# Performance work log

Hardware: AMD Instinct MI355X
Metric: run time of the kernel (lower is better)

Reference implementation:

```python
import math
import jax, jax.numpy as jnp
import numpy as np

B, S, HIDDEN = 1, 8192, 2048
NUM_HEADS = 16
HEAD_DIM = HIDDEN // NUM_HEADS
NUM_FW = 4
FW_DIM = HIDDEN // NUM_FW
D_H = FW_DIM  # inter_multi = 1.0
WINDOW = 256
CHUNK = 2048
ROPE_THETA = 500000.0
BASE_LR_INV = float(np.log(np.expm1(0.001)))  # inv_softplus(1e-3)


def rms_norm(x, w, eps=1e-6):
    return x * jax.lax.rsqrt(jnp.mean(x * x, axis=-1, keepdims=True) + eps) * w


def apply_rope(q, k, theta):
    D = q.shape[-1]
    inv = 1.0 / (theta ** (jnp.arange(0, D, 2, dtype=jnp.float32) / D))
    t = jnp.arange(q.shape[1], dtype=jnp.float32)
    f = t[:, None] * inv[None, :]  # [S, D/2]
    cos = jnp.cos(f)[None, :, None, :]
    sin = jnp.sin(f)[None, :, None, :]
    def ap(x):
        x1, x2 = jnp.split(x, 2, axis=-1)
        return jnp.concatenate([x1 * cos - x2 * sin, x2 * cos + x1 * sin], axis=-1)
    return ap(q), ap(k)


def sliding_window_attn(q, k, v, window):
    # q,k,v: [B,S,H,D]; causal window of `window` tokens incl. self (flash (window-1, 0))
    B_, S_, H_, D_ = q.shape
    W = window
    nc = S_ // W
    def blk(x):
        return x.transpose(0, 2, 1, 3).reshape(B_, H_, nc, W, D_)
    qb, kb, vb = blk(q), blk(k), blk(v)
    pad = jnp.zeros((B_, H_, 1, W, D_), q.dtype)
    k2 = jnp.concatenate([jnp.concatenate([pad, kb[:, :, :-1]], 2), kb], 3)  # [B,H,nc,2W,D]
    v2 = jnp.concatenate([jnp.concatenate([pad, vb[:, :, :-1]], 2), vb], 3)
    r = jnp.arange(W)[:, None]
    j = jnp.arange(2 * W)[None, :]
    base = (j >= r + 1) & (j <= W + r)  # causal + within-window
    keypos = (jnp.arange(nc)[:, None, None] - 1) * W + j[None]
    mask = base[None] & (keypos >= 0)  # [nc,W,2W]
    scores = jnp.einsum('bhnqd,bhnkd->bhnqk', qb, k2) * (1.0 / math.sqrt(D_))
    scores = jnp.where(mask[None, None], scores, -jnp.inf)
    p = jax.nn.softmax(scores, axis=-1)
    o = jnp.einsum('bhnqk,bhnkd->bhnqd', p, v2)
    return o.reshape(B_, H_, S_, D_).transpose(0, 2, 1, 3)


def ttt_swiglu(fq, fk, fv, l0, l1, l2, w0, w1, w2, chunk):
    # fq/fk/fv: [BN,S,d]; l*: [BN,S,1]; w0,w2: [BN,dh,d]; w1: [BN,d,dh]
    BN, S_, d = fq.shape
    nc = S_ // chunk
    def ch(x):
        return x.reshape(BN, nc, chunk, x.shape[-1]).transpose(1, 0, 2, 3)
    xs = (ch(fq), ch(fk), ch(fv), ch(l0), ch(l1), ch(l2))
    def step(carry, x):
        w0c, w1c, w2c = carry
        qi, ki, vi, lr0, lr1, lr2 = x
        # apply current fast weights to chunk queries (SwiGLU MLP)
        o = jnp.einsum('bch,boh->bco',
                       jax.nn.silu(jnp.einsum('bcd,bhd->bch', qi, w0c)) * jnp.einsum('bcd,bhd->bch', qi, w2c),
                       w1c)
        # manual gradient of dot-product TTT loss L = -sum(v * f(k))
        g = jnp.einsum('bcd,bhd->bch', ki, w0c)
        hm = jnp.einsum('bcd,bhd->bch', ki, w2c)
        sg = jax.nn.sigmoid(g)
        silu_g = g * sg
        hid = silu_g * hm
        dhid = jnp.einsum('bco,boh->bch', vi, w1c)
        dhm = dhid * silu_g
        dg = dhid * hm
        dgp = dg * (sg * (1.0 + g * (1.0 - sg)))  # silu backprop
        w0n = w0c + jnp.einsum('bch,bcd->bhd', dgp * lr0, ki)
        w2n = w2c + jnp.einsum('bch,bcd->bhd', dhm * lr2, ki)
        w1n = w1c + jnp.einsum('bco,bch->boh', vi * lr1, hid)
        return (w0n, w1n, w2n), o
    _, outs = jax.lax.scan(step, (w0, w1, w2), xs)
    return outs.transpose(1, 0, 2, 3).reshape(BN, S_, d)


def setup_inputs():
    key = jax.random.key(0)
    ks = jax.random.split(key, 8)
    h = HIDDEN
    return {
        'hidden_states': jax.random.normal(ks[0], (B, S, h), jnp.float32),
        'qkv_w': jax.random.normal(ks[1], (3 * h, h), jnp.float32) * 0.02,
        'q_norm_w': jnp.ones((h,), jnp.float32),
        'k_norm_w': jnp.ones((h,), jnp.float32),
        'qk_scale': jnp.ones((h, 2), jnp.float32),
        'qk_offset': jnp.zeros((h, 2), jnp.float32),
        'lr_w': jax.random.normal(ks[2], (3 * NUM_FW, h), jnp.float32) * 0.02,
        'lr_b': jnp.zeros((3 * NUM_FW,), jnp.float32),
        'w0': jax.random.normal(ks[3], (NUM_FW, D_H, FW_DIM), jnp.float32) / math.sqrt(FW_DIM),
        'w1': jax.random.normal(ks[4], (NUM_FW, FW_DIM, D_H), jnp.float32) / math.sqrt(D_H),
        'w2': jax.random.normal(ks[5], (NUM_FW, D_H, FW_DIM), jnp.float32) / math.sqrt(FW_DIM),
        'ttt_norm_w': jnp.ones((FW_DIM,), jnp.float32),
        'o_proj_w': jax.random.normal(ks[6], (h, h), jnp.float32) * 0.02,
    }


def reference(hidden_states, qkv_w, q_norm_w, k_norm_w, qk_scale, qk_offset,
              lr_w, lr_b, w0, w1, w2, ttt_norm_w, o_proj_w):
    qkv = hidden_states @ qkv_w.T
    q, k, v = jnp.split(qkv, 3, axis=-1)
    q = rms_norm(q, q_norm_w)
    k = rms_norm(k, k_norm_w)
    # rescale q/k for the fast-weight path
    fq = q * qk_scale[:, 0] + qk_offset[:, 0]
    fk = k * qk_scale[:, 1] + qk_offset[:, 1]
    fv = v
    # windowed RoPE attention path
    qh = q.reshape(B, S, NUM_HEADS, HEAD_DIM)
    kh = k.reshape(B, S, NUM_HEADS, HEAD_DIM)
    vh = v.reshape(B, S, NUM_HEADS, HEAD_DIM)
    qh, kh = apply_rope(qh, kh, ROPE_THETA)
    attn_o = sliding_window_attn(qh, kh, vh, WINDOW).reshape(B, S, HIDDEN)
    # fast-weight (TTT) path: silu + per-head l2-norm on q/k
    fq = jax.nn.silu(fq).reshape(B, S, NUM_FW, FW_DIM)
    fk = jax.nn.silu(fk).reshape(B, S, NUM_FW, FW_DIM)
    fv = jax.nn.silu(fv).reshape(B, S, NUM_FW, FW_DIM)
    fq = fq / jnp.maximum(jnp.linalg.norm(fq, axis=-1, keepdims=True), 1e-12)
    fk = fk / jnp.maximum(jnp.linalg.norm(fk, axis=-1, keepdims=True), 1e-12)
    def flat(x):
        return x.transpose(0, 2, 1, 3).reshape(B * NUM_FW, S, FW_DIM)
    # per-token learning rates (mamba parameterization)
    lr = jax.nn.softplus(hidden_states @ lr_w.T + lr_b + BASE_LR_INV)  # [B,S,3*NH]
    l0, l1, l2 = jnp.split(lr, 3, axis=-1)
    def flat_lr(x):
        return x.transpose(0, 2, 1).reshape(B * NUM_FW, S, 1)
    def bcast(w):
        return jnp.broadcast_to(w[None], (B,) + w.shape).reshape(B * NUM_FW, w.shape[1], w.shape[2])
    o_fast = ttt_swiglu(flat(fq), flat(fk), flat(fv),
                        flat_lr(l0), flat_lr(l1), flat_lr(l2),
                        bcast(w0), bcast(w1), bcast(w2), CHUNK)
    o_fast = rms_norm(o_fast.reshape(B, NUM_FW, S, FW_DIM), ttt_norm_w)
    o_fast = o_fast.transpose(0, 2, 1, 3).reshape(B, S, HIDDEN)
    return (attn_o + o_fast) @ o_proj_w.T
```

## Files before the change

kernel.cpp:

```cpp
#include <hip/hip_runtime.h>
#include <hip/hip_bf16.h>

typedef __hip_bfloat16 bf16;
typedef __bf16 bft;
typedef bft bf16x8 __attribute__((ext_vector_type(8)));
typedef bft bf16x4 __attribute__((ext_vector_type(4)));
typedef float f32x4 __attribute__((ext_vector_type(4)));

#define S_LEN 8192
#define HID   2048
#define QKV3  6144
#define NH    16
#define HD    128
#define NFW   4
#define FD    512
#define CHUNK_LEN 2048
#define NCHUNK 4
#define BASE_LR_INV (-6.9072552f)
#define QKP 136
#define VSP 72
#define PSP 76

__device__ __forceinline__ float bf2f(bf16 x){ return __bfloat162float(x); }
__device__ __forceinline__ bf16  f2bf(float x){ return __float2bfloat16(x); }
__device__ __forceinline__ float sigm(float x){ return 1.f/(1.f+__expf(-x)); }
__device__ __forceinline__ float siluf(float x){ return x/(1.f+__expf(-x)); }
__device__ __forceinline__ float wave_sum(float v){
  #pragma unroll
  for(int off=32; off; off>>=1) v += __shfl_xor(v, off, 64);
  return v;
}

template<int ROWS, typename T>
__device__ __forceinline__ void stage(const T* __restrict__ src, long ld,
                                      bft* dst, int tid)
{
  if constexpr (sizeof(T) == 2) {
    const int lane = tid & 63, wv = tid >> 6;
    #pragma unroll
    for (int i = 0; i < ROWS/64; ++i) {
      const int r0 = wv*16 + i*64;
      const int row = r0 + (lane >> 2);
      const int g = (lane & 3) ^ ((row >> 1) & 3);
      const bft* gp = (const bft*)src + (size_t)row*ld + g*8;
      bft* lp = dst + (size_t)r0*32;
      __builtin_amdgcn_global_load_lds(
          (const __attribute__((address_space(1))) void*)gp,
          (__attribute__((address_space(3))) void*)lp, 16, 0, 0);
    }
  } else {
    #pragma unroll
    for (int i = 0; i < ROWS/64; ++i) {
      const int e = tid + i*256;
      const int row = e >> 2, c = e & 3;
      const int g = c ^ ((row >> 1) & 3);
      const float* sp = (const float*)src + (size_t)row*ld + g*8;
      const float4 v0 = *(const float4*)sp;
      const float4 v1 = *(const float4*)(sp + 4);
      bf16x8 b;
      b[0]=(bft)v0.x; b[1]=(bft)v0.y; b[2]=(bft)v0.z; b[3]=(bft)v0.w;
      b[4]=(bft)v1.x; b[5]=(bft)v1.y; b[6]=(bft)v1.z; b[7]=(bft)v1.w;
      *(bf16x8*)(dst + (size_t)row*32 + c*8) = b;
    }
  }
}

template<int BM,int BN,int EPI, typename TA, typename TB>
__global__ __launch_bounds__(256) void mgemm_k(
    const TA* __restrict__ A, const TB* __restrict__ B, void* __restrict__ Cv,
    bft* __restrict__ Ct, int K, long lda, long ldb, long ldc,
    long sA, long sB, long sC)
{
  constexpr int AM = BM/32, AN = BN/32;
  __shared__ __align__(16) bft As[BM*32];
  __shared__ __align__(16) bft Bs[BN*32];
  const int tid = threadIdx.x;
  const int z = blockIdx.z;
  A += (size_t)z * sA;
  B += (size_t)z * sB;
  const size_t m0 = (size_t)blockIdx.y * BM, n0 = (size_t)blockIdx.x * BN;
  const int wv = tid >> 6, lane = tid & 63;
  const int wm = (wv & 1) * (BM/2), wn = (wv >> 1) * (BN/2);
  const int fr = lane & 15;
  const int fsw = ((lane >> 4) ^ ((fr >> 1) & 3)) * 8;

  f32x4 acc[AM][AN];
  #pragma unroll
  for (int i=0;i<AM;i++)
    #pragma unroll
    for (int j=0;j<AN;j++) acc[i][j] = (f32x4){0.f,0.f,0.f,0.f};

  const TA* Ab = A + m0*lda;
  const TB* Bb = B + n0*ldb;
  for (int kt = 0; kt < K; kt += 32) {
    __syncthreads();
    stage<BM>(Ab + kt, lda, As, tid);
    stage<BN>(Bb + kt, ldb, Bs, tid);
    __syncthreads();
    bf16x8 af[AM], bfv[AN];
    #pragma unroll
    for (int mi=0; mi<AM; mi++)
      af[mi] = *(const bf16x8*)(As + (size_t)(wm + mi*16 + fr)*32 + fsw);
    #pragma unroll
    for (int ni=0; ni<AN; ni++)
      bfv[ni] = *(const bf16x8*)(Bs + (size_t)(wn + ni*16 + fr)*32 + fsw);
    #pragma unroll
    for (int mi=0; mi<AM; mi++)
      #pragma unroll
      for (int ni=0; ni<AN; ni++)
        acc[mi][ni] = __builtin_amdgcn_mfma_f32_16x16x32_bf16(af[mi], bfv[ni], acc[mi][ni], 0, 0, 0);
  }

  const int er = (lane >> 4) * 4;
  const int ec = lane & 15;
  #pragma unroll
  for (int mi=0; mi<AM; mi++){
    #pragma unroll
    for (int ni=0; ni<AN; ni++){
      #pragma unroll
      for (int r=0; r<4; r++){
        size_t row = m0 + wm + mi*16 + er + r;
        size_t col = n0 + wn + ni*16 + ec;
        size_t idx = (size_t)z*sC + row*ldc + col;
        float v = acc[mi][ni][r];
        if constexpr (EPI == 0){
          ((bft*)Cv)[idx] = (bft)v;
        } else if constexpr (EPI == 1){
          ((float*)Cv)[idx] = v;
        } else {
          float nv = ((float*)Cv)[idx] + v;
          ((float*)Cv)[idx] = nv;
          if (Ct) Ct[(size_t)z*FD*FD + col*FD + row] = (bft)nv;
        }
      }
    }
  }
}

template<int BM,int BN,int EPI, typename TA, typename TB>
static inline void mgemm(hipStream_t st, const TA* A, const TB* B, void* C, bft* Ct,
    int M, int N, int K, long lda, long ldb, long ldc,
    int batch, long sA, long sB, long sC)
{
  dim3 g(N/BN, M/BM, batch);
  mgemm_k<BM,BN,EPI,TA,TB><<<g, 256, 0, st>>>(A, B, C, Ct, K, lda, ldb, ldc, sA, sB, sC);
}

__device__ __forceinline__ void stage8(const bft* __restrict__ src, long ld,
                                       bft* dst, int tid)
{
  const int lane = tid & 63, wv = tid >> 6;
  #pragma unroll
  for (int i = 0; i < 2; ++i) {
    const int r0 = wv*16 + i*128;
    const int row = r0 + (lane >> 2);
    const int g = (lane & 3) ^ ((row >> 1) & 3);
    const bft* gp = src + (size_t)row*ld + g*8;
    bft* lp = dst + (size_t)r0*32;
    __builtin_amdgcn_global_load_lds(
        (const __attribute__((address_space(1))) void*)gp,
        (__attribute__((address_space(3))) void*)lp, 16, 0, 0);
  }
}

template<int EPI>
__global__ __launch_bounds__(512, 2) void mgemm8_k(
    const bft* __restrict__ A, const bft* __restrict__ B, void* __restrict__ Cv,
    int K, long lda, long ldb, long ldc)
{
  __shared__ __align__(16) bft As[4][256*32];
  __shared__ __align__(16) bft Bs[4][256*32];
  const int tid = threadIdx.x;

  const int gx = (int)gridDim.x;
  const int nwg = (int)(gridDim.x * gridDim.y);
  int lin = (int)(blockIdx.y * gridDim.x + blockIdx.x);
  if ((nwg & 7) == 0) lin = (lin & 7) * (nwg >> 3) + (lin >> 3);
  const size_t m0 = (size_t)(lin / gx) * 256;
  const size_t n0 = (size_t)(lin % gx) * 256;

  const int wv = tid >> 6, lane = tid & 63;
  const int wm = (wv & 1) * 128, wn = (wv >> 1) * 64;
  const int fr = lane & 15;
  const int fsw = ((lane >> 4) ^ ((fr >> 1) & 3)) * 8;

  f32x4 acc[8][4];
  #pragma unroll
  for (int i=0;i<8;i++)
    #pragma unroll
    for (int j=0;j<4;j++) acc[i][j] = (f32x4){0.f,0.f,0.f,0.f};

  const bft* Ab = A + m0*lda;
  const bft* Bb = B + n0*ldb;
  const int NS = K >> 5;

  stage8(Ab,      lda, As[0], tid);
  stage8(Bb,      ldb, Bs[0], tid);
  stage8(Ab + 32, lda, As[1], tid);
  stage8(Bb + 32, ldb, Bs[1], tid);

  auto compute = [&](int s){
    const bft* Ap = As[s & 3];
    const bft* Bp = Bs[s & 3];
    bf16x8 af[8], bv[4];
    #pragma unroll
    for (int mi=0; mi<8; mi++)
      af[mi] = *(const bf16x8*)(Ap + (size_t)(wm + mi*16 + fr)*32 + fsw);
    #pragma unroll
    for (int ni=0; ni<4; ni++)
      bv[ni] = *(const bf16x8*)(Bp + (size_t)(wn + ni*16 + fr)*32 + fsw);
    __builtin_amdgcn_s_setprio(1);
    #pragma unroll
    for (int mi=0; mi<8; mi++)
      #pragma unroll
      for (int ni=0; ni<4; ni++)
        acc[mi][ni] = __builtin_amdgcn_mfma_f32_16x16x32_bf16(af[mi], bv[ni], acc[mi][ni], 0, 0, 0);
    __builtin_amdgcn_s_setprio(0);
  };

  for (int s = 0; s < NS - 2; ++s) {
    const int kt = (s + 2) * 32;
    stage8(Ab + kt, lda, As[(s+2)&3], tid);
    stage8(Bb + kt, ldb, Bs[(s+2)&3], tid);
    asm volatile("s_waitcnt vmcnt(8)" ::: "memory");
    __builtin_amdgcn_s_barrier();
    asm volatile("" ::: "memory");
    compute(s);
  }
  asm volatile("s_waitcnt vmcnt(4)" ::: "memory");
  __builtin_amdgcn_s_barrier();
  asm volatile("" ::: "memory");
  compute(NS - 2);
  asm volatile("s_waitcnt vmcnt(0)" ::: "memory");
  __builtin_amdgcn_s_barrier();
  asm volatile("" ::: "memory");
  compute(NS - 1);

  const int er = (lane >> 4) * 4;
  const int ec = lane & 15;
  #pragma unroll
  for (int mi=0; mi<8; mi++){
    #pragma unroll
    for (int ni=0; ni<4; ni++){
      #pragma unroll
      for (int r=0; r<4; r++){
        size_t row = m0 + wm + mi*16 + er + r;
        size_t col = n0 + wn + ni*16 + ec;
        size_t idx = row*ldc + col;
        float v = acc[mi][ni][r];
        if constexpr (EPI == 0) ((bft*)Cv)[idx] = (bft)v;
        else                    ((float*)Cv)[idx] = v;
      }
    }
  }
}

template<int EPI>
static inline void mgemm8(hipStream_t st, const bft* A, const bft* B, void* C,
                          int M, int N, int K, long lda, long ldb, long ldc)
{
  dim3 g(N/256, M/256, 1);
  mgemm8_k<EPI><<<g, 512, 0, st>>>(A, B, C, K, lda, ldb, ldc);
}

__global__ __launch_bounds__(256) void cvt_k(const float* __restrict__ s,
    bft* __restrict__ d)
{
  size_t i = ((size_t)blockIdx.x*256 + threadIdx.x) * 8;
  const float4 v0 = *(const float4*)(s + i);
  const float4 v1 = *(const float4*)(s + i + 4);
  bf16x8 b;
  b[0]=(bft)v0.x; b[1]=(bft)v0.y; b[2]=(bft)v0.z; b[3]=(bft)v0.w;
  b[4]=(bft)v1.x; b[5]=(bft)v1.y; b[6]=(bft)v1.z; b[7]=(bft)v1.w;
  *(bf16x8*)(d + i) = b;
}

__global__ __launch_bounds__(256) void tr_k(const bft* __restrict__ in,
    bft* __restrict__ out, long ldin, long sIn, long sOut)
{
  __shared__ __align__(16) bft t[64][72];
  const int c0 = blockIdx.x*64, r0 = blockIdx.y*64;
  in  += (size_t)blockIdx.z * sIn;
  out += (size_t)blockIdx.z * sOut;
  const int tid = threadIdx.x;
  #pragma unroll
  for (int i=0;i<2;i++){
    int e = tid + i*256;
    int r = e >> 3, c8 = (e & 7) * 8;
    *(bf16x8*)&t[r][c8] = *(const bf16x8*)(in + (size_t)(r0+r)*ldin + c0 + c8);
  }
  __syncthreads();
  #pragma unroll
  for (int i=0;i<2;i++){
    int e = tid + i*256;
    int c = e >> 3, r8 = (e & 7) * 8;
    bf16x8 v;
    #pragma unroll
    for (int j=0;j<8;j++) v[j] = t[r8+j][c];
    *(bf16x8*)(out + (size_t)(c0+c)*CHUNK_LEN + r0 + r8) = v;
  }
}

__global__ __launch_bounds__(256) void tcw1_k(const float* __restrict__ w1,
    bft* __restrict__ w1tb)
{
  size_t idx = (size_t)blockIdx.x*256 + threadIdx.x;
  int z = (int)(idx >> 18);
  int h = (int)((idx >> 9) & 511);
  int o = (int)(idx & 511);
  w1tb[idx] = (bft)w1[(size_t)z*FD*FD + (size_t)o*FD + h];
}

__global__ __launch_bounds__(256) void vt_k(const bf16* __restrict__ qkv,
    bft* __restrict__ vT)
{
  __shared__ __align__(16) bft t[64*QKP];
  const int s0 = blockIdx.x * 64;
  const int h  = blockIdx.y;
  const int tid = threadIdx.x;
  #pragma unroll
  for (int i=0;i<4;i++){
    int e = tid + i*256;
    int rr = e >> 4, doff = (e & 15) * 8;
    *(bf16x8*)(t + rr*QKP + doff) =
        *(const bf16x8*)((const bft*)qkv + (size_t)(s0+rr)*QKV3 + 2*HID + h*HD + doff);
  }
  __syncthreads();
  #pragma unroll
  for (int it=0; it<4; it++){
    int d = (tid >> 3) + it*32;
    int so8 = (tid & 7) * 8;
    bf16x8 v;
    #pragma unroll
    for (int j=0;j<8;j++) v[j] = t[(so8+j)*QKP + d];
    *(bf16x8*)(vT + ((size_t)(h*HD + d))*S_LEN + s0 + so8) = v;
  }
}

__global__ void rope_k(float* __restrict__ rc, float* __restrict__ rs){
  int pos = blockIdx.x, d = threadIdx.x;
  float inv = 1.f / powf(500000.0f, (float)d * (1.0f/64.0f));
  float ang = (float)pos * inv;
  rc[pos*64+d] = cosf(ang);
  rs[pos*64+d] = sinf(ang);
}

__global__ __launch_bounds__(256) void lr_k(const float* __restrict__ hidden,
    const float* __restrict__ lr_w, const float* __restrict__ lr_b,
    float* __restrict__ lro)
{
  __shared__ float hrow[HID];
  __shared__ float red[4][12];
  int s = blockIdx.x, tid = threadIdx.x;
  for(int i=0;i<HID/256;i++) hrow[tid+256*i] = hidden[(size_t)s*HID + tid + 256*i];
  __syncthreads();
  float part[12];
  #pragma unroll
  for(int o=0;o<12;o++) part[o]=0.f;
  for(int i=0;i<HID/256;i++){
    int j = tid + 256*i;
    float h = hrow[j];
    #pragma unroll
    for(int o=0;o<12;o++) part[o] += h * lr_w[o*HID + j];
  }
  int lane = tid & 63, w = tid >> 6;
  #pragma unroll
  for(int o=0;o<12;o++){
    float v = wave_sum(part[o]);
    if(lane==0) red[w][o] = v;
  }
  __syncthreads();
  if(tid < 12){
    float v = red[0][tid]+red[1][tid]+red[2][tid]+red[3][tid] + lr_b[tid] + BASE_LR_INV;
    float sp = (v > 20.f) ? v : log1pf(expf(v));
    lro[s*12 + tid] = sp;
  }
}

__global__ __launch_bounds__(256) void e2a_k(
    bf16* __restrict__ qkv,
    const float* __restrict__ qnw, const float* __restrict__ knw)
{
  __shared__ float red[8];
  int s = blockIdx.x, tid = threadIdx.x;
  int lane = tid & 63, w = tid >> 6;
  float qv[8], kv[8];
  float sq = 0.f, sk = 0.f;
  size_t base = (size_t)s*QKV3;
  #pragma unroll
  for(int i=0;i<8;i++){
    int j = tid*8 + i;
    qv[i] = bf2f(qkv[base + j]);
    kv[i] = bf2f(qkv[base + HID + j]);
    sq += qv[i]*qv[i]; sk += kv[i]*kv[i];
  }
  sq = wave_sum(sq); sk = wave_sum(sk);
  if(lane==0){ red[w] = sq; red[4+w] = sk; }
  __syncthreads();
  float rq = rsqrtf((red[0]+red[1]+red[2]+red[3])*(1.f/HID) + 1e-6f);
  float rk = rsqrtf((red[4]+red[5]+red[6]+red[7])*(1.f/HID) + 1e-6f);
  #pragma unroll
  for(int i=0;i<8;i++){
    int j = tid*8 + i;
    qkv[base + j]       = f2bf(qv[i]*rq*qnw[j]);
    qkv[base + HID + j] = f2bf(kv[i]*rk*knw[j]);
  }
}

__global__ __launch_bounds__(256) void e2b_k(
    bf16* __restrict__ qkv,
    const float* __restrict__ qks, const float* __restrict__ qko)
{
  int s = blockIdx.x, tid = threadIdx.x;
  size_t base = (size_t)s*QKV3;
  float a[8], b[8], vv[8];
  float ga = 0.f, gb2 = 0.f;
  #pragma unroll
  for(int i=0;i<8;i++){
    int j = tid*8 + i;
    float qn = bf2f(qkv[base + j]);
    float kn = bf2f(qkv[base + HID + j]);
    float v  = bf2f(qkv[base + 2*HID + j]);
    a[i] = siluf(qn*qks[2*j]   + qko[2*j]);
    b[i] = siluf(kn*qks[2*j+1] + qko[2*j+1]);
    vv[i] = siluf(v);
    ga += a[i]*a[i]; gb2 += b[i]*b[i];
  }
  ga = wave_sum(ga); gb2 = wave_sum(gb2);
  float iq = 1.f / fmaxf(sqrtf(ga), 1e-12f);
  float ik = 1.f / fmaxf(sqrtf(gb2), 1e-12f);
  #pragma unroll
  for(int i=0;i<8;i++){
    int j = tid*8 + i;
    qkv[base + j]         = f2bf(a[i]*iq);
    qkv[base + HID + j]   = f2bf(b[i]*ik);
    qkv[base + 2*HID + j] = f2bf(vv[i]);
  }
}

__global__ __launch_bounds__(256) void attn_k(
    const bf16* __restrict__ qkv, const bft* __restrict__ vT,
    const float* __restrict__ rc, const float* __restrict__ rs,
    float* __restrict__ attn)
{
  __shared__ __align__(16) bft Qs[64*QKP];
  __shared__ __align__(16) bft Ks[64*QKP];
  __shared__ __align__(16) bft Vs[128*VSP];
  __shared__ __align__(16) bft Ps[64*PSP];
  const int head = blockIdx.x >> 7;
  const int Q0 = (blockIdx.x & 127) * 64;
  const int tid = threadIdx.x;
  const int hb = head * HD;
  const int lane = tid & 63;
  const int wm = (tid >> 6) * 16;
  const int fr = lane & 15, fko = (lane >> 4) * 8;
  const int rbase = (lane >> 4) * 4;

  #pragma unroll
  for(int i=0;i<16;i++){
    int e = tid + i*256;
    int rr = e >> 6, d = e & 63;
    int qpos = Q0 + rr;
    size_t b = (size_t)qpos*QKV3 + hb;
    float x1 = bf2f(qkv[b + d]);
    float x2 = bf2f(qkv[b + d + 64]);
    float c = rc[qpos*64 + d], sn = rs[qpos*64 + d];
    Qs[rr*QKP + d]      = (bft)(x1*c - x2*sn);
    Qs[rr*QKP + d + 64] = (bft)(x2*c + x1*sn);
  }
  __syncthreads();
  bf16x8 qf[4];
  #pragma unroll
  for (int kk=0;kk<4;kk++)
    qf[kk] = *(const bf16x8*)(Qs + (wm+fr)*QKP + kk*32 + fko);

  f32x4 Ot[8];
  #pragma unroll
  for (int i=0;i<8;i++) Ot[i] = (f32x4){0.f,0.f,0.f,0.f};
  float m4[4], l4[4];
  #pragma unroll
  for (int r=0;r<4;r++){ m4[r] = -INFINITY; l4[r] = 0.f; }

  for (int kt=0; kt<5; kt++){
    const int kb = Q0 - 256 + kt*64;
    if (kb < 0) continue;
    __syncthreads();
    #pragma unroll
    for(int i=0;i<16;i++){
      int e = tid + i*256;
      int rr = e >> 6, d = e & 63;
      int kpos = kb + rr;
      size_t b = (size_t)kpos*QKV3 + HID + hb;
      float x1 = bf2f(qkv[b + d]);
      float x2 = bf2f(qkv[b + d + 64]);
      float c = rc[kpos*64 + d], sn = rs[kpos*64 + d];
      Ks[rr*QKP + d]      = (bft)(x1*c - x2*sn);
      Ks[rr*QKP + d + 64] = (bft)(x2*c + x1*sn);
    }
    {
      int d = tid >> 1, koff = (tid & 1) * 32;
      const bft* vrow = vT + ((size_t)(hb + d))*S_LEN + kb + koff;
      bft* lrow = Vs + d*VSP + koff;
      #pragma unroll
      for (int j8=0;j8<4;j8++)
        *(bf16x8*)(lrow + j8*8) = *(const bf16x8*)(vrow + j8*8);
    }
    __syncthreads();

    f32x4 st[4];
    #pragma unroll
    for (int nt=0;nt<4;nt++){
      f32x4 acc = (f32x4){0.f,0.f,0.f,0.f};
      #pragma unroll
      for (int kk=0;kk<4;kk++){
        bf16x8 kf = *(const bf16x8*)(Ks + (nt*16+fr)*QKP + kk*32 + fko);
        acc = __builtin_amdgcn_mfma_f32_16x16x32_bf16(qf[kk], kf, acc, 0, 0, 0);
      }
      st[nt] = acc;
    }

    float pv[4][4];
    #pragma unroll
    for (int r=0;r<4;r++){
      int qpos = Q0 + wm + rbase + r;
      float sm[4];
      float mx = -INFINITY;
      #pragma unroll
      for (int nt=0;nt<4;nt++){
        int kpos = kb + nt*16 + fr;
        bool valid = (kpos > qpos - 256) && (kpos <= qpos);
        float s = valid ? st[nt][r] * 0.088388347648318447f : -INFINITY;
        sm[nt] = s;
        mx = fmaxf(mx, s);
      }
      mx = fmaxf(mx, __shfl_xor(mx, 1, 64));
      mx = fmaxf(mx, __shfl_xor(mx, 2, 64));
      mx = fmaxf(mx, __shfl_xor(mx, 4, 64));
      mx = fmaxf(mx, __shfl_xor(mx, 8, 64));
      float mnew = fmaxf(m4[r], mx);
      float alpha = (mnew == -INFINITY) ? 1.f : __expf(m4[r] - mnew);
      float ps = 0.f;
      #pragma unroll
      for (int nt=0;nt<4;nt++){
        float p = (sm[nt] == -INFINITY) ? 0.f : __expf(sm[nt] - mnew);
        pv[nt][r] = p;
        ps += p;
      }
      ps += __shfl_xor(ps, 1, 64);
      ps += __shfl_xor(ps, 2, 64);
      ps += __shfl_xor(ps, 4, 64);
      ps += __shfl_xor(ps, 8, 64);
      l4[r] = l4[r]*alpha + ps;
      m4[r] = mnew;
      #pragma unroll
      for (int ct=0;ct<8;ct++) Ot[ct][r] *= alpha;
    }

    #pragma unroll
    for (int r=0;r<4;r++){
      int row = wm + rbase + r;
      #pragma unroll
      for (int nt=0;nt<4;nt++)
        Ps[row*PSP + nt*16 + fr] = (bft)pv[nt][r];
    }
    bf16x8 af[2];
    #pragma unroll
    for (int kk=0;kk<2;kk++){
      const bft* pp = Ps + (wm+fr)*PSP + kk*32 + fko;
      bf16x4 lo = *(const bf16x4*)pp;
      bf16x4 hi = *(const bf16x4*)(pp+4);
      bf16x8 a;
      #pragma unroll
      for (int j=0;j<4;j++){ a[j]=lo[j]; a[j+4]=hi[j]; }
      af[kk]=a;
    }
    #pragma unroll
    for (int ct=0;ct<8;ct++)
      #pragma unroll
      for (int kk=0;kk<2;kk++){
        bf16x8 bv = *(const bf16x8*)(Vs + (ct*16+fr)*VSP + kk*32 + fko);
        Ot[ct] = __builtin_amdgcn_mfma_f32_16x16x32_bf16(af[kk], bv, Ot[ct], 0, 0, 0);
      }
  }

  #pragma unroll
  for (int r=0;r<4;r++){
    float invl = 1.f / l4[r];
    int qpos = Q0 + wm + rbase + r;
    size_t ob = (size_t)qpos*HID + hb;
    #pragma unroll
    for (int ct=0;ct<8;ct++)
      attn[ob + ct*16 + fr] = Ot[ct][r] * invl;
  }
}

__global__ __launch_bounds__(256) void e3_k(
    const bf16* __restrict__ g, const bf16* __restrict__ hm,
    bf16* __restrict__ qg, const bf16* __restrict__ qm,
    bf16* __restrict__ hid)
{
  size_t idx = (size_t)blockIdx.x*256 + threadIdx.x;
  float opre = siluf(bf2f(qg[idx])) * bf2f(qm[idx]);
  hid[idx] = f2bf(siluf(bf2f(g[idx])) * bf2f(hm[idx]));
  qg[idx]  = f2bf(opre);
}

__global__ __launch_bounds__(256) void e4_k(
    bf16* __restrict__ g, bf16* __restrict__ hm, bf16* __restrict__ dhid,
    const bf16* __restrict__ qkv, const float* __restrict__ lrb, int cbase)
{
  size_t idx = (size_t)blockIdx.x*256 + threadIdx.x;
  int h  = (int)(idx >> 20);
  int ci = (int)((idx >> 9) & 2047);
  int d  = (int)(idx & 511);
  int s  = cbase + ci;
  float l0  = lrb[s*12 + h];
  float l1  = lrb[s*12 + 4 + h];
  float l2v = lrb[s*12 + 8 + h];
  float gg = bf2f(g[idx]), hv = bf2f(hm[idx]), dh = bf2f(dhid[idx]);
  float sg = sigm(gg);
  float silu_g = gg * sg;
  float dhm = dh * silu_g;
  float dg  = dh * hv;
  float dgp = dg * (sg * (1.f + gg * (1.f - sg)));
  float fvv = bf2f(qkv[(size_t)s*QKV3 + 2*HID + h*FD + d]);
  g[idx]    = f2bf(dgp * l0);
  hm[idx]   = f2bf(dhm * l2v);
  dhid[idx] = f2bf(fvv * l1);
}

__global__ __launch_bounds__(256) void e5_k(const float* __restrict__ attn,
    const bf16* __restrict__ ofc, const float* __restrict__ tnw,
    bf16* __restrict__ qkv, int cbase)
{
  int ci = blockIdx.x, tid = threadIdx.x;
  int s = cbase + ci;
  int lane = tid & 63, w = tid >> 6;
  float o[8]; float ss = 0.f;
  size_t ob = ((size_t)w*CHUNK_LEN + ci)*FD + (size_t)lane*8;
  #pragma unroll
  for(int i=0;i<8;i++){ o[i] = bf2f(ofc[ob+i]); ss += o[i]*o[i]; }
  ss = wave_sum(ss);
  float inv = rsqrtf(ss*(1.f/FD) + 1e-6f);
  size_t xb = (size_t)s*QKV3 + w*FD + (size_t)lane*8;
  size_t ab = (size_t)s*HID  + w*FD + (size_t)lane*8;
  #pragma unroll
  for(int i=0;i<8;i++){
    int d = lane*8 + i;
    qkv[xb+i] = f2bf(attn[ab+i] + o[i]*inv*tnw[d]);
  }
}

extern "C" void kernel_launch(void* const* d_in, const int* in_sizes, int n_in,
                              void* d_out, int out_size, void* d_ws, size_t ws_size,
                              hipStream_t stream)
{
  (void)in_sizes; (void)n_in; (void)out_size;
  const float* hidden   = (const float*)d_in[0];
  const float* qkv_w    = (const float*)d_in[1];
  const float* q_norm_w = (const float*)d_in[2];
  const float* k_norm_w = (const float*)d_in[3];
  const float* qk_scale = (const float*)d_in[4];
  const float* qk_off   = (const float*)d_in[5];
  const float* lr_w     = (const float*)d_in[6];
  const float* lr_b     = (const float*)d_in[7];
  const float* w0_in    = (const float*)d_in[8];
  const float* w1_in    = (const float*)d_in[9];
  const float* w2_in    = (const float*)d_in[10];
  const float* ttt_nw   = (const float*)d_in[11];
  const float* o_proj   = (const float*)d_in[12];
  float* out = (float*)d_out;

  char* p = (char*)d_ws;
  auto alloc = [&](size_t n){ char* r = p; p += (n + 255) & ~(size_t)255; return (void*)r; };

  bf16*  qkv   = (bf16*) alloc((size_t)S_LEN*QKV3*sizeof(bf16));
  float* lrb   = (float*)alloc((size_t)S_LEN*12*sizeof(float));
  float* rc    = (float*)alloc((size_t)S_LEN*64*sizeof(float));
  float* rs    = (float*)alloc((size_t)S_LEN*64*sizeof(float));
  float* w0s   = (float*)alloc((size_t)NFW*FD*FD*sizeof(float));
  float* w1s   = (float*)alloc((size_t)NFW*FD*FD*sizeof(float));
  float* w2s   = (float*)alloc((size_t)NFW*FD*FD*sizeof(float));
  bft*   w1tb  = (bft*)  alloc((size_t)NFW*FD*FD*sizeof(bft));
  bf16*  gb    = (bf16*) alloc((size_t)NFW*CHUNK_LEN*FD*sizeof(bf16));
  bf16*  hmb   = (bf16*) alloc((size_t)NFW*CHUNK_LEN*FD*sizeof(bf16));
  bf16*  qgb   = (bf16*) alloc((size_t)NFW*CHUNK_LEN*FD*sizeof(bf16));
  bf16*  qmb   = (bf16*) alloc((size_t)NFW*CHUNK_LEN*FD*sizeof(bf16));
  bf16*  hidb  = (bf16*) alloc((size_t)NFW*CHUNK_LEN*FD*sizeof(bf16));
  bf16*  ofc   = (bf16*) alloc((size_t)NFW*CHUNK_LEN*FD*sizeof(bf16));
  bft*   fkT   = (bft*)  alloc((size_t)NFW*FD*CHUNK_LEN*sizeof(bft));
  bft*   hidT  = (bft*)  alloc((size_t)NFW*FD*CHUNK_LEN*sizeof(bft));
  bft*   a2T   = (bft*)  alloc((size_t)NFW*FD*CHUNK_LEN*sizeof(bft));
  bft*   a1T   = (bft*)  alloc((size_t)NFW*FD*CHUNK_LEN*sizeof(bft));

  if ((size_t)(p - (char*)d_ws) > ws_size) return;

  bft* hidden_bf = (bft*)gb;
  bft* qkvw_bf   = (bft*)fkT;
  bft* vT        = (bft*)fkT;
  bft* opw_bf    = (bft*)hidb;

  float* attn = out;

  hipMemcpyAsync(w0s, w0_in, (size_t)NFW*FD*FD*sizeof(float), hipMemcpyDeviceToDevice, stream);
  hipMemcpyAsync(w1s, w1_in, (size_t)NFW*FD*FD*sizeof(float), hipMemcpyDeviceToDevice, stream);
  hipMemcpyAsync(w2s, w2_in, (size_t)NFW*FD*FD*sizeof(float), hipMemcpyDeviceToDevice, stream);

  rope_k<<<S_LEN, 64, 0, stream>>>(rc, rs);
  lr_k<<<S_LEN, 256, 0, stream>>>(hidden, lr_w, lr_b, lrb);
  tcw1_k<<<NFW*FD*FD/256, 256, 0, stream>>>(w1_in, w1tb);
  cvt_k<<<(S_LEN*HID)/2048, 256, 0, stream>>>(hidden, hidden_bf);
  cvt_k<<<(QKV3*HID)/2048, 256, 0, stream>>>(qkv_w, qkvw_bf);

  mgemm8<0>(stream, hidden_bf, qkvw_bf, (void*)qkv, S_LEN, QKV3, HID, HID, HID, QKV3);

  e2a_k<<<S_LEN, 256, 0, stream>>>(qkv, q_norm_w, k_norm_w);
  vt_k<<<dim3(S_LEN/64, NH), 256, 0, stream>>>(qkv, vT);
  attn_k<<<NH*128, 256, 0, stream>>>(qkv, vT, rc, rs, attn);
  e2b_k<<<S_LEN, 256, 0, stream>>>(qkv, qk_scale, qk_off);

  const long sW  = (long)FD*FD;
  const long sCh = (long)CHUNK_LEN*FD;
  const long sT  = (long)FD*CHUNK_LEN;
  const int  NEL = NFW*CHUNK_LEN*FD/256;
  const dim3 tg(FD/64, CHUNK_LEN/64, NFW);

  for(int c=0; c<NCHUNK; c++){
    const bft* fqc = (const bft*)qkv + (size_t)c*CHUNK_LEN*QKV3;
    const bft* fkc = fqc + HID;
    const bft* fvc = fqc + 2*HID;
    mgemm<128,128,0>(stream, fkc, w0s, gb,  (bft*)nullptr, CHUNK_LEN, FD, FD, QKV3, FD, FD, NFW, FD, sW, sCh);
    mgemm<128,128,0>(stream, fkc, w2s, hmb, (bft*)nullptr, CHUNK_LEN, FD, FD, QKV3, FD, FD, NFW, FD, sW, sCh);
    mgemm<128,128,0>(stream, fqc, w0s, qgb, (bft*)nullptr, CHUNK_LEN, FD, FD, QKV3, FD, FD, NFW, FD, sW, sCh);
    mgemm<128,128,0>(stream, fqc, w2s, qmb, (bft*)nullptr, CHUNK_LEN, FD, FD, QKV3, FD, FD, NFW, FD, sW, sCh);
    e3_k<<<NEL, 256, 0, stream>>>(gb, hmb, qgb, qmb, hidb);
    mgemm<128,128,0>(stream, (const bft*)qgb, w1s, ofc, (bft*)nullptr, CHUNK_LEN, FD, FD, FD, FD, FD, NFW, sCh, sW, sCh);
    mgemm<128,128,0>(stream, fvc, (const bft*)w1tb, qmb, (bft*)nullptr, CHUNK_LEN, FD, FD, QKV3, FD, FD, NFW, FD, sW, sCh);
    e4_k<<<NEL, 256, 0, stream>>>(gb, hmb, qmb, qkv, lrb, c*CHUNK_LEN);
    tr_k<<<tg, 256, 0, stream>>>(fkc,              fkT,        QKV3, FD,  sT);
    tr_k<<<tg, 256, 0, stream>>>((const bft*)hidb, hidT,       FD,   sCh, sT);
    tr_k<<<tg, 256, 0, stream>>>((const bft*)gb,   (bft*)qgb,  FD,   sCh, sT);
    tr_k<<<tg, 256, 0, stream>>>((const bft*)hmb,  a2T,        FD,   sCh, sT);
    tr_k<<<tg, 256, 0, stream>>>((const bft*)qmb,  a1T,        FD,   sCh, sT);
    mgemm<64,64,2>(stream, (const bft*)qgb, fkT,  w0s, (bft*)nullptr, FD, FD, CHUNK_LEN, CHUNK_LEN, CHUNK_LEN, FD, NFW, sT, sT, sW);
    mgemm<64,64,2>(stream, a2T,             fkT,  w2s, (bft*)nullptr, FD, FD, CHUNK_LEN, CHUNK_LEN, CHUNK_LEN, FD, NFW, sT, sT, sW);
    mgemm<64,64,2>(stream, a1T,             hidT, w1s, w1tb,          FD, FD, CHUNK_LEN, CHUNK_LEN, CHUNK_LEN, FD, NFW, sT, sT, sW);
    e5_k<<<CHUNK_LEN, 256, 0, stream>>>(attn, ofc, ttt_nw, qkv, c*CHUNK_LEN);
  }

  cvt_k<<<(HID*HID)/2048, 256, 0, stream>>>(o_proj, opw_bf);
  mgemm8<1>(stream, (const bft*)qkv, opw_bf, out, S_LEN, HID, HID, QKV3, HID, HID);
}
```

Measured before the change: 1.703 ms.

## Pipeline TTT GEMM loads with 4-stage LDS ring and keep bf16 weight copies

Replaces the single-buffered, double-barrier mgemm loop with a 4-slot LDS ring that prefetches two K-steps ahead using global_load_lds, explicit vmcnt waits and one barrier per step, and raises MFMA issue priority. Fast weights are now also kept as bf16 copies, refreshed in the weight-update epilogue. This lets every GEMM take the async bf16 staging path instead of loading fp32 and converting in registers. The cost is extra bf16 stores in the update epilogue, more LDS per block, and three small conversion kernels.

```diff
diff --git a/kernel.cpp b/kernel.cpp
--- a/kernel.cpp
+++ b/kernel.cpp
@@ -31,49 +31,43 @@
   return v;
 }
 
-template<int ROWS, typename T>
-__device__ __forceinline__ void stage(const T* __restrict__ src, long ld,
+template<int N>
+__device__ __forceinline__ void waitcnt_vm(){
+  static_assert(N==0||N==2||N==4||N==8, "unsupported vmcnt");
+  if constexpr (N==0)      asm volatile("s_waitcnt vmcnt(0)" ::: "memory");
+  else if constexpr (N==2) asm volatile("s_waitcnt vmcnt(2)" ::: "memory");
+  else if constexpr (N==4) asm volatile("s_waitcnt vmcnt(4)" ::: "memory");
+  else                     asm volatile("s_waitcnt vmcnt(8)" ::: "memory");
+}
+
+template<int ROWS>
+__device__ __forceinline__ void stage(const bft* __restrict__ src, long ld,
                                       bft* dst, int tid)
 {
-  if constexpr (sizeof(T) == 2) {
-    const int lane = tid & 63, wv = tid >> 6;
-    #pragma unroll
-    for (int i = 0; i < ROWS/64; ++i) {
-      const int r0 = wv*16 + i*64;
-      const int row = r0 + (lane >> 2);
-      const int g = (lane & 3) ^ ((row >> 1) & 3);
-      const bft* gp = (const bft*)src + (size_t)row*ld + g*8;
-      bft* lp = dst + (size_t)r0*32;
-      __builtin_amdgcn_global_load_lds(
-          (const __attribute__((address_space(1))) void*)gp,
-          (__attribute__((address_space(3))) void*)lp, 16, 0, 0);
-    }
-  } else {
-    #pragma unroll
-    for (int i = 0; i < ROWS/64; ++i) {
-      const int e = tid + i*256;
-      const int row = e >> 2, c = e & 3;
-      const int g = c ^ ((row >> 1) & 3);
-      const float* sp = (const float*)src + (size_t)row*ld + g*8;
-      const float4 v0 = *(const float4*)sp;
-      const float4 v1 = *(const float4*)(sp + 4);
-      bf16x8 b;
-      b[0]=(bft)v0.x; b[1]=(bft)v0.y; b[2]=(bft)v0.z; b[3]=(bft)v0.w;
-      b[4]=(bft)v1.x; b[5]=(bft)v1.y; b[6]=(bft)v1.z; b[7]=(bft)v1.w;
-      *(bf16x8*)(dst + (size_t)row*32 + c*8) = b;
-    }
-  }
-}
-
-template<int BM,int BN,int EPI, typename TA, typename TB>
+  const int lane = tid & 63, wv = tid >> 6;
+  #pragma unroll
+  for (int i = 0; i < ROWS/64; ++i) {
+    const int r0 = wv*16 + i*64;
+    const int row = r0 + (lane >> 2);
+    const int g = (lane & 3) ^ ((row >> 1) & 3);
+    const bft* gp = src + (size_t)row*ld + g*8;
+    bft* lp = dst + (size_t)r0*32;
+    __builtin_amdgcn_global_load_lds(
+        (const __attribute__((address_space(1))) void*)gp,
+        (__attribute__((address_space(3))) void*)lp, 16, 0, 0);
+  }
+}
+
+template<int BM,int BN,int EPI>
 __global__ __launch_bounds__(256) void mgemm_k(
-    const TA* __restrict__ A, const TB* __restrict__ B, void* __restrict__ Cv,
-    bft* __restrict__ Ct, int K, long lda, long ldb, long ldc,
-    long sA, long sB, long sC)
+    const bft* __restrict__ A, const bft* __restrict__ B, void* __restrict__ Cv,
+    bft* __restrict__ Cd, bft* __restrict__ Ct, int K,
+    long lda, long ldb, long ldc, long sA, long sB, long sC)
 {
   constexpr int AM = BM/32, AN = BN/32;
-  __shared__ __align__(16) bft As[BM*32];
-  __shared__ __align__(16) bft Bs[BN*32];
+  constexpr int LPS = BM/64 + BN/64;
+  __shared__ __align__(16) bft As[4][BM*32];
+  __shared__ __align__(16) bft Bs[4][BN*32];
   const int tid = threadIdx.x;
   const int z = blockIdx.z;
   A += (size_t)z * sA;
@@ -90,26 +84,51 @@
     #pragma unroll
     for (int j=0;j<AN;j++) acc[i][j] = (f32x4){0.f,0.f,0.f,0.f};
 
-  const TA* Ab = A + m0*lda;
-  const TB* Bb = B + n0*ldb;
-  for (int kt = 0; kt < K; kt += 32) {
-    __syncthreads();
-    stage<BM>(Ab + kt, lda, As, tid);
-    stage<BN>(Bb + kt, ldb, Bs, tid);
-    __syncthreads();
+  const bft* Ab = A + m0*lda;
+  const bft* Bb = B + n0*ldb;
+  const int NS = K >> 5;
+
+  stage<BM>(Ab,      lda, As[0], tid);
+  stage<BN>(Bb,      ldb, Bs[0], tid);
+  stage<BM>(Ab + 32, lda, As[1], tid);
+  stage<BN>(Bb + 32, ldb, Bs[1], tid);
+
+  auto compute = [&](int s){
+    const bft* Ap = As[s & 3];
+    const bft* Bp = Bs[s & 3];
     bf16x8 af[AM], bfv[AN];
     #pragma unroll
     for (int mi=0; mi<AM; mi++)
-      af[mi] = *(const bf16x8*)(As + (size_t)(wm + mi*16 + fr)*32 + fsw);
+      af[mi] = *(const bf16x8*)(Ap + (size_t)(wm + mi*16 + fr)*32 + fsw);
     #pragma unroll
     for (int ni=0; ni<AN; ni++)
-      bfv[ni] = *(const bf16x8*)(Bs + (size_t)(wn + ni*16 + fr)*32 + fsw);
+      bfv[ni] = *(const bf16x8*)(Bp + (size_t)(wn + ni*16 + fr)*32 + fsw);
+    __builtin_amdgcn_s_setprio(1);
     #pragma unroll
     for (int mi=0; mi<AM; mi++)
       #pragma unroll
       for (int ni=0; ni<AN; ni++)
         acc[mi][ni] = __builtin_amdgcn_mfma_f32_16x16x32_bf16(af[mi], bfv[ni], acc[mi][ni], 0, 0, 0);
-  }
+    __builtin_amdgcn_s_setprio(0);
+  };
+
+  for (int s = 0; s < NS - 2; ++s) {
+    const int kt = (s + 2) * 32;
+    stage<BM>(Ab + kt, lda, As[(s+2)&3], tid);
+    stage<BN>(Bb + kt, ldb, Bs[(s+2)&3], tid);
+    waitcnt_vm<2*LPS>();
+    __builtin_amdgcn_s_barrier();
+    asm volatile("" ::: "memory");
+    compute(s);
+  }
+  waitcnt_vm<LPS>();
+  __builtin_amdgcn_s_barrier();
+  asm volatile("" ::: "memory");
+  compute(NS - 2);
+  waitcnt_vm<0>();
+  __builtin_amdgcn_s_barrier();
+  asm volatile("" ::: "memory");
+  compute(NS - 1);
 
   const int er = (lane >> 4) * 4;
   const int ec = lane & 15;
@@ -130,6 +149,7 @@
         } else {
           float nv = ((float*)Cv)[idx] + v;
           ((float*)Cv)[idx] = nv;
+          Cd[idx] = (bft)nv;
           if (Ct) Ct[(size_t)z*FD*FD + col*FD + row] = (bft)nv;
         }
       }
@@ -137,13 +157,13 @@
   }
 }
 
-template<int BM,int BN,int EPI, typename TA, typename TB>
-static inline void mgemm(hipStream_t st, const TA* A, const TB* B, void* C, bft* Ct,
-    int M, int N, int K, long lda, long ldb, long ldc,
+template<int BM,int BN,int EPI>
+static inline void mgemm(hipStream_t st, const bft* A, const bft* B, void* C,
+    bft* Cd, bft* Ct, int M, int N, int K, long lda, long ldb, long ldc,
     int batch, long sA, long sB, long sC)
 {
   dim3 g(N/BN, M/BM, batch);
-  mgemm_k<BM,BN,EPI,TA,TB><<<g, 256, 0, st>>>(A, B, C, Ct, K, lda, ldb, ldc, sA, sB, sC);
+  mgemm_k<BM,BN,EPI><<<g, 256, 0, st>>>(A, B, C, Cd, Ct, K, lda, ldb, ldc, sA, sB, sC);
 }
 
 __device__ __forceinline__ void stage8(const bft* __restrict__ src, long ld,
@@ -682,6 +702,9 @@
   float* w1s   = (float*)alloc((size_t)NFW*FD*FD*sizeof(float));
   float* w2s   = (float*)alloc((size_t)NFW*FD*FD*sizeof(float));
   bft*   w1tb  = (bft*)  alloc((size_t)NFW*FD*FD*sizeof(bft));
+  bft*   w0b   = (bft*)  alloc((size_t)NFW*FD*FD*sizeof(bft));
+  bft*   w1b   = (bft*)  alloc((size_t)NFW*FD*FD*sizeof(bft));
+  bft*   w2b   = (bft*)  alloc((size_t)NFW*FD*FD*sizeof(bft));
   bf16*  gb    = (bf16*) alloc((size_t)NFW*CHUNK_LEN*FD*sizeof(bf16));
   bf16*  hmb   = (bf16*) alloc((size_t)NFW*CHUNK_LEN*FD*sizeof(bf16));
   bf16*  qgb   = (bf16*) alloc((size_t)NFW*CHUNK_LEN*FD*sizeof(bf16));
@@ -709,6 +732,9 @@
   rope_k<<<S_LEN, 64, 0, stream>>>(rc, rs);
   lr_k<<<S_LEN, 256, 0, stream>>>(hidden, lr_w, lr_b, lrb);
   tcw1_k<<<NFW*FD*FD/256, 256, 0, stream>>>(w1_in, w1tb);
+  cvt_k<<<(NFW*FD*FD)/2048, 256, 0, stream>>>(w0_in, w0b);
+  cvt_k<<<(NFW*FD*FD)/2048, 256, 0, stream>>>(w1_in, w1b);
+  cvt_k<<<(NFW*FD*FD)/2048, 256, 0, stream>>>(w2_in, w2b);
   cvt_k<<<(S_LEN*HID)/2048, 256, 0, stream>>>(hidden, hidden_bf);
   cvt_k<<<(QKV3*HID)/2048, 256, 0, stream>>>(qkv_w, qkvw_bf);
 
@@ -729,22 +755,22 @@
     const bft* fqc = (const bft*)qkv + (size_t)c*CHUNK_LEN*QKV3;
     const bft* fkc = fqc + HID;
     const bft* fvc = fqc + 2*HID;
-    mgemm<128,128,0>(stream, fkc, w0s, gb,  (bft*)nullptr, CHUNK_LEN, FD, FD, QKV3, FD, FD, NFW, FD, sW, sCh);
-    mgemm<128,128,0>(stream, fkc, w2s, hmb, (bft*)nullptr, CHUNK_LEN, FD, FD, QKV3, FD, FD, NFW, FD, sW, sCh);
-    mgemm<128,128,0>(stream, fqc, w0s, qgb, (bft*)nullptr, CHUNK_LEN, FD, FD, QKV3, FD, FD, NFW, FD, sW, sCh);
-    mgemm<128,128,0>(stream, fqc, w2s, qmb, (bft*)nullptr, CHUNK_LEN, FD, FD, QKV3, FD, FD, NFW, FD, sW, sCh);
+    mgemm<128,128,0>(stream, fkc, w0b, gb,  nullptr, nullptr, CHUNK_LEN, FD, FD, QKV3, FD, FD, NFW, FD, sW, sCh);
+    mgemm<128,128,0>(stream, fkc, w2b, hmb, nullptr, nullptr, CHUNK_LEN, FD, FD, QKV3, FD, FD, NFW, FD, sW, sCh);
+    mgemm<128,128,0>(stream, fqc, w0b, qgb, nullptr, nullptr, CHUNK_LEN, FD, FD, QKV3, FD, FD, NFW, FD, sW, sCh);
+    mgemm<128,128,0>(stream, fqc, w2b, qmb, nullptr, nullptr, CHUNK_LEN, FD, FD, QKV3, FD, FD, NFW, FD, sW, sCh);
     e3_k<<<NEL, 256, 0, stream>>>(gb, hmb, qgb, qmb, hidb);
-    mgemm<128,128,0>(stream, (const bft*)qgb, w1s, ofc, (bft*)nullptr, CHUNK_LEN, FD, FD, FD, FD, FD, NFW, sCh, sW, sCh);
-    mgemm<128,128,0>(stream, fvc, (const bft*)w1tb, qmb, (bft*)nullptr, CHUNK_LEN, FD, FD, QKV3, FD, FD, NFW, FD, sW, sCh);
+    mgemm<128,128,0>(stream, (const bft*)qgb, w1b, ofc, nullptr, nullptr, CHUNK_LEN, FD, FD, FD, FD, FD, NFW, sCh, sW, sCh);
+    mgemm<128,128,0>(stream, fvc, (const bft*)w1tb, qmb, nullptr, nullptr, CHUNK_LEN, FD, FD, QKV3, FD, FD, NFW, FD, sW, sCh);
     e4_k<<<NEL, 256, 0, stream>>>(gb, hmb, qmb, qkv, lrb, c*CHUNK_LEN);
     tr_k<<<tg, 256, 0, stream>>>(fkc,              fkT,        QKV3, FD,  sT);
     tr_k<<<tg, 256, 0, stream>>>((const bft*)hidb, hidT,       FD,   sCh, sT);
     tr_k<<<tg, 256, 0, stream>>>((const bft*)gb,   (bft*)qgb,  FD,   sCh, sT);
     tr_k<<<tg, 256, 0, stream>>>((const bft*)hmb,  a2T,        FD,   sCh, sT);
     tr_k<<<tg, 256, 0, stream>>>((const bft*)qmb,  a1T,        FD,   sCh, sT);
-    mgemm<64,64,2>(stream, (const bft*)qgb, fkT,  w0s, (bft*)nullptr, FD, FD, CHUNK_LEN, CHUNK_LEN, CHUNK_LEN, FD, NFW, sT, sT, sW);
-    mgemm<64,64,2>(stream, a2T,             fkT,  w2s, (bft*)nullptr, FD, FD, CHUNK_LEN, CHUNK_LEN, CHUNK_LEN, FD, NFW, sT, sT, sW);
-    mgemm<64,64,2>(stream, a1T,             hidT, w1s, w1tb,          FD, FD, CHUNK_LEN, CHUNK_LEN, CHUNK_LEN, FD, NFW, sT, sT, sW);
+    mgemm<64,64,2>(stream, (const bft*)qgb, fkT,  w0s, w0b, nullptr, FD, FD, CHUNK_LEN, CHUNK_LEN, CHUNK_LEN, FD, NFW, sT, sT, sW);
+    mgemm<64,64,2>(stream, a2T,             fkT,  w2s, w2b, nullptr, FD, FD, CHUNK_LEN, CHUNK_LEN, CHUNK_LEN, FD, NFW, sT, sT, sW);
+    mgemm<64,64,2>(stream, a1T,             hidT, w1s, w1b, w1tb,    FD, FD, CHUNK_LEN, CHUNK_LEN, CHUNK_LEN, FD, NFW, sT, sT, sW);
     e5_k<<<CHUNK_LEN, 256, 0, stream>>>(attn, ofc, ttt_nw, qkv, c*CHUNK_LEN);
   }
 
```

Measured after the change: 1.578 ms. 1.08x faster.
